# Kernel optimization log

Measured on AMD Instinct MI355X. Metric: run time of the kernel, lower is better.

## Reference

```python
import jax, jax.numpy as jnp
from jax import lax
import numpy as np

N, D, K, T, E, S = 2048, 128, 16, 16, 8192, 256
GAMMA, SIGMA, TEMP, EPS = 0.1, 1.0, 1.0, 1e-10


def _xavier(k, out_d, in_d):
    lim = (6.0 / (in_d + out_d)) ** 0.5
    return jax.random.uniform(k, (out_d, in_d), minval=-lim, maxval=lim, dtype=jnp.float32)


def setup_inputs() -> dict:
    key = jax.random.key(0)
    ks = jax.random.split(key, 24)
    inp = {
        'edges': jax.random.randint(ks[0], (T, E, 2), 0, N, dtype=jnp.int32),
        'subject_idx': 3,
        'eps_phi': jax.random.normal(ks[1], (T, N, D), dtype=jnp.float32),
        'eps_beta': jax.random.normal(ks[2], (T, K, D), dtype=jnp.float32),
        'u_gumbel': jax.random.uniform(ks[3], (T, 2 * E, K), dtype=jnp.float32),
        'alpha_mean_emb': jax.random.normal(ks[4], (S, D), dtype=jnp.float32),
        'alpha_std_emb': jax.random.normal(ks[5], (S, D), dtype=jnp.float32),
        'W_s2phi': _xavier(ks[6], N * D, D), 'b_s2phi': jnp.zeros((N * D,), jnp.float32),
        'W_s2beta': _xavier(ks[7], K * D, D), 'b_s2beta': jnp.zeros((K * D,), jnp.float32),
        'W_bmean': _xavier(ks[8], D, D), 'b_bmean': jnp.zeros((D,), jnp.float32),
        'W_bstd': _xavier(ks[9], D, D), 'b_bstd': jnp.zeros((D,), jnp.float32),
        'W_pmean': _xavier(ks[10], D, D), 'b_pmean': jnp.zeros((D,), jnp.float32),
        'W_pstd': _xavier(ks[11], D, D), 'b_pstd': jnp.zeros((D,), jnp.float32),
        'W_pi': _xavier(ks[12], K, D),
        'Wih_n': 0.1 * jax.random.normal(ks[13], (3 * D, 2 * D), dtype=jnp.float32),
        'Whh_n': 0.1 * jax.random.normal(ks[14], (3 * D, D), dtype=jnp.float32),
        'bih_n': jnp.zeros((3 * D,), jnp.float32), 'bhh_n': jnp.zeros((3 * D,), jnp.float32),
        'Wih_c': 0.1 * jax.random.normal(ks[15], (3 * D, 2 * D), dtype=jnp.float32),
        'Whh_c': 0.1 * jax.random.normal(ks[16], (3 * D, D), dtype=jnp.float32),
        'bih_c': jnp.zeros((3 * D,), jnp.float32), 'bhh_c': jnp.zeros((3 * D,), jnp.float32),
        'W_dec': _xavier(ks[17], N, D),
    }
    return inp


def _gru(x, h, Wih, Whh, bih, bhh):
    # torch nn.GRU single-step cell (gate order r, z, n)
    gi = x @ Wih.T + bih
    gh = h @ Whh.T + bhh
    i_r, i_z, i_n = jnp.split(gi, 3, axis=-1)
    h_r, h_z, h_n = jnp.split(gh, 3, axis=-1)
    r = jax.nn.sigmoid(i_r + h_r)
    z = jax.nn.sigmoid(i_z + h_z)
    n = jnp.tanh(i_n + r * h_n)
    return (1.0 - z) * n + z * h


def _kld_gauss(m1, s1, m2, s2):
    # KL(N(m1,s1) || N(m2,s2)), s2 scalar
    return 0.5 * jnp.sum(2.0 * (jnp.log(s2) - jnp.log(s1)) + (s1 ** 2 + (m1 - m2) ** 2) / (s2 ** 2) - 1.0)


def reference(edges, subject_idx, eps_phi, eps_beta, u_gumbel,
              alpha_mean_emb, alpha_std_emb, W_s2phi, b_s2phi, W_s2beta, b_s2beta,
              W_bmean, b_bmean, W_bstd, b_bstd, W_pmean, b_pmean, W_pstd, b_pstd,
              W_pi, Wih_n, Whh_n, bih_n, bhh_n, Wih_c, Whh_c, bih_c, bhh_c, W_dec):
    a_m = alpha_mean_emb[subject_idx]
    a_s = jax.nn.softplus(alpha_std_emb[subject_idx])
    kld_alpha = _kld_gauss(a_m, a_s, jnp.zeros_like(a_m), 1.0)
    phi0 = (a_m @ W_s2phi.T + b_s2phi).reshape(N, D)
    beta0 = (a_m @ W_s2beta.T + b_s2beta).reshape(K, D)

    def step(carry, xs):
        h_phi, h_beta, phi_prior, beta_prior = carry
        e_t, ep, eb, u = xs
        w = jnp.concatenate([e_t[:, 0], e_t[:, 1]])  # [2E]
        c = jnp.concatenate([e_t[:, 1], e_t[:, 0]])  # [2E]
        h_phi = _gru(jnp.concatenate([phi_prior, phi_prior], -1), h_phi, Wih_n, Whh_n, bih_n, bhh_n)
        h_beta = _gru(jnp.concatenate([beta_prior, beta_prior], -1), h_beta, Wih_c, Whh_c, bih_c, bhh_c)
        beta_mean = h_beta @ W_bmean.T + b_bmean
        beta_std = jax.nn.softplus(h_beta @ W_bstd.T + b_bstd)
        phi_mean = h_phi @ W_pmean.T + b_pmean
        phi_std = jax.nn.softplus(h_phi @ W_pstd.T + b_pstd)
        beta_s = beta_mean + beta_std * eb  # [K, D]
        phi_s = phi_mean + phi_std * ep     # [N, D]
        logits_q = (phi_s[w] * phi_s[c]) @ W_pi.T        # [2E, K] posterior logits
        log_post = jax.nn.log_softmax(logits_q, axis=-1)
        post = jnp.exp(log_post)
        log_prior = jax.nn.log_softmax(phi_s[w] @ beta_s.T, axis=-1)  # p(z|w)
        g = -jnp.log(-jnp.log(u + EPS) + EPS)  # gumbel noise
        z = jax.nn.softmax((logits_q + g) / TEMP, axis=-1)  # soft gumbel-softmax sample
        recon_logp = jax.nn.log_softmax((z @ beta_s) @ W_dec.T, axis=-1)  # [2E, N]
        nll = -jnp.sum(jnp.take_along_axis(recon_logp, c[:, None], axis=1))
        kld_z = jnp.sum(post * (log_post - log_prior))
        kld_beta = _kld_gauss(beta_mean, beta_std, beta_prior, GAMMA)
        kld_phi = _kld_gauss(phi_mean, phi_std, phi_prior, SIGMA)
        return (h_phi, h_beta, phi_s, beta_s), jnp.stack([nll, kld_z, kld_beta, kld_phi])

    carry0 = (jnp.zeros((N, D), jnp.float32), jnp.zeros((K, D), jnp.float32), phi0, beta0)
    _, per_t = lax.scan(step, carry0, (edges, eps_phi, eps_beta, u_gumbel))
    sums = per_t.sum(axis=0)  # [nll, kld_z, kld_beta, kld_phi]
    cnt = jnp.float32(T * 2 * E)
    out = jnp.stack([sums[0], sums[1], T * kld_alpha, sums[2], sums[3]]) / cnt
    return out  # [nll, kld_z, kld_alpha, kld_beta, kld_phi]
```

## Files before the change

kernel.cpp:

```cpp
#include <hip/hip_runtime.h>

#define NN 2048
#define DD 128
#define KK 16
#define TT 16
#define EE 8192
#define TWOE 16384
#define CNT 262144.0f

#define LOG2E 1.4426950408889634f
#define LN2   0.6931471805599453f

__device__ __forceinline__ float exp2_(float x) { return __builtin_amdgcn_exp2f(x); }
__device__ __forceinline__ float log2_(float x) { return __builtin_amdgcn_logf(x); }
__device__ __forceinline__ float expf_(float x) { return exp2_(x * LOG2E); }
__device__ __forceinline__ float logf_(float x) { return log2_(x) * LN2; }
__device__ __forceinline__ float sigmoidf_(float x) { return 1.f / (1.f + expf_(-x)); }
__device__ __forceinline__ float softplusf_(float x) { return fmaxf(x, 0.f) + logf_(1.f + expf_(-fabsf(x))); }
__device__ __forceinline__ float tanhf_(float x) { return 1.f - 2.f / (1.f + expf_(2.f * x)); }

#define D4(a,b) ((a).x*(b).x + (a).y*(b).y + (a).z*(b).z + (a).w*(b).w)

__launch_bounds__(256)
__global__ void init_kernel(const float* __restrict__ Wih_n, const float* __restrict__ Whh_n,
                            const float* __restrict__ Wih_c, const float* __restrict__ Whh_c,
                            const float* __restrict__ W_pmean, const float* __restrict__ W_pstd,
                            const float* __restrict__ W_bmean, const float* __restrict__ W_bstd,
                            float* __restrict__ Bg_n, float* __restrict__ Bg_c,
                            float* __restrict__ Bms_n, float* __restrict__ Bms_c,
                            float* __restrict__ hphiA, float* __restrict__ hbetaA,
                            const float* __restrict__ amE, const float* __restrict__ asE,
                            const int* __restrict__ sidx, float* __restrict__ a_m,
                            float* __restrict__ acc)
{
    if (blockIdx.x == 1024) {
        __shared__ float red[128];
        int d = threadIdx.x;
        if (d < 128) {
            int s = sidx[0];
            float am = amE[s*128 + d];
            float as = softplusf_(asE[s*128 + d]);
            a_m[d] = am;
            red[d] = -logf_(as) + 0.5f*(as*as + am*am) - 0.5f;
        }
        __syncthreads();
        for (int st = 64; st > 0; st >>= 1) { if (d < st) red[d] += red[d + st]; __syncthreads(); }
        if (d == 0) acc[2] = red[0];
        return;
    }
    int idx = blockIdx.x * 256 + threadIdx.x;
    hphiA[idx] = 0.f;
    if (idx < 2048) hbetaA[idx] = 0.f;
    if (idx < 2) { acc[idx] = 0.f; acc[idx + 3] = 0.f; }
    if (idx < 98304) {
        int r = idx;
        if (r < 49152) { int j = r >> 7, k2 = r & 127; Bg_n[r] = Wih_n[j*256 + k2] + Wih_n[j*256 + 128 + k2]; }
        else Bg_n[r] = Whh_n[r - 49152];
    } else if (idx < 196608) {
        int r = idx - 98304;
        if (r < 49152) { int j = r >> 7, k2 = r & 127; Bg_c[r] = Wih_c[j*256 + k2] + Wih_c[j*256 + 128 + k2]; }
        else Bg_c[r] = Whh_c[r - 49152];
    } else if (idx < 229376) {
        int r = idx - 196608;
        Bms_n[r] = (r < 16384) ? W_pmean[r] : W_pstd[r - 16384];
    } else {
        int r = idx - 229376;
        Bms_c[r] = (r < 16384) ? W_bmean[r] : W_bstd[r - 16384];
    }
}

__launch_bounds__(256)
__global__ void phi0_kernel(const float* __restrict__ Wp, const float* __restrict__ bp,
                            const float* __restrict__ Wb, const float* __restrict__ bb,
                            const float* __restrict__ a_m, float* __restrict__ phi0, float* __restrict__ beta0)
{
    int wid = threadIdx.x >> 6, l = threadIdx.x & 63;
    long long row = (long long)blockIdx.x * 4 + wid;
    const float* W; const float* b; float* o; long long r = row;
    if (row < 262144) { W = Wp; b = bp; o = phi0; }
    else { W = Wb; b = bb; o = beta0; r = row - 262144; }
    const float* wr = W + r * 128;
    float acc = a_m[l] * wr[l] + a_m[64 + l] * wr[64 + l];
    #pragma unroll
    for (int m = 32; m >= 1; m >>= 1) acc += __shfl_xor(acc, m);
    if (l == 0) o[r] = acc + b[r];
}

__launch_bounds__(256)
__global__ void gru_kernel(const float* __restrict__ phiPrior, const float* __restrict__ betaPrior,
                           const float* __restrict__ hPhiOld, float* __restrict__ hPhiNew,
                           const float* __restrict__ hBetaOld, float* __restrict__ hBetaNew,
                           const float* __restrict__ Bg_n, const float* __restrict__ Bg_c,
                           const float* __restrict__ bih_n, const float* __restrict__ bhh_n,
                           const float* __restrict__ bih_c, const float* __restrict__ bhh_c)
{
    __shared__ float Xs[32][64];
    __shared__ float Hs[32][64];
    __shared__ float Ws[32][192];
    int bx = blockIdx.x;
    const float* X; const float* Hold; float* Hnew; const float* Bg; const float* bih; const float* bhh;
    int m0, M, j0;
    if (bx < 128) {
        m0 = (bx >> 2) * 64; j0 = (bx & 3) * 32; M = 2048;
        X = phiPrior; Hold = hPhiOld; Hnew = hPhiNew; Bg = Bg_n; bih = bih_n; bhh = bhh_n;
    } else {
        m0 = 0; j0 = (bx - 128) * 32; M = 16;
        X = betaPrior; Hold = hBetaOld; Hnew = hBetaNew; Bg = Bg_c; bih = bih_c; bhh = bhh_c;
    }
    int tid = threadIdx.x;
    int j  = tid & 31;
    int rr = tid >> 5;
    float acc[6][8] = {};
    int srow = tid >> 3;
    int skq  = (tid & 7) * 4;
    for (int k0 = 0; k0 < 128; k0 += 32) {
        #pragma unroll
        for (int h2 = 0; h2 < 2; ++h2) {
            int row = srow + 32 * h2;
            int grow = m0 + row;
            float4 xv = make_float4(0.f,0.f,0.f,0.f), hv = xv;
            if (grow < M) {
                xv = *(const float4*)(X    + (size_t)grow*128 + k0 + skq);
                hv = *(const float4*)(Hold + (size_t)grow*128 + k0 + skq);
            }
            Xs[skq+0][row] = xv.x; Xs[skq+1][row] = xv.y; Xs[skq+2][row] = xv.z; Xs[skq+3][row] = xv.w;
            Hs[skq+0][row] = hv.x; Hs[skq+1][row] = hv.y; Hs[skq+2][row] = hv.z; Hs[skq+3][row] = hv.w;
        }
        #pragma unroll
        for (int h6 = 0; h6 < 6; ++h6) {
            int rowIdx = srow + 32 * h6;
            int g = rowIdx >> 5, jj2 = rowIdx & 31;
            float4 wv = *(const float4*)(Bg + (size_t)(g*128 + j0 + jj2)*128 + k0 + skq);
            Ws[skq+0][rowIdx] = wv.x; Ws[skq+1][rowIdx] = wv.y; Ws[skq+2][rowIdx] = wv.z; Ws[skq+3][rowIdx] = wv.w;
        }
        __syncthreads();
        #pragma unroll
        for (int kk = 0; kk < 32; ++kk) {
            float xa[8], ha[8];
            *(float4*)&xa[0] = *(const float4*)&Xs[kk][rr*8];
            *(float4*)&xa[4] = *(const float4*)&Xs[kk][rr*8+4];
            *(float4*)&ha[0] = *(const float4*)&Hs[kk][rr*8];
            *(float4*)&ha[4] = *(const float4*)&Hs[kk][rr*8+4];
            #pragma unroll
            for (int g = 0; g < 3; ++g) {
                float wv = Ws[kk][g*32 + j];
                #pragma unroll
                for (int i = 0; i < 8; ++i) acc[g][i] = fmaf(xa[i], wv, acc[g][i]);
            }
            #pragma unroll
            for (int g = 3; g < 6; ++g) {
                float wv = Ws[kk][g*32 + j];
                #pragma unroll
                for (int i = 0; i < 8; ++i) acc[g][i] = fmaf(ha[i], wv, acc[g][i]);
            }
        }
        __syncthreads();
    }
    float bi_r = bih[j0 + j], bi_z = bih[128 + j0 + j], bi_n = bih[256 + j0 + j];
    float bh_r = bhh[j0 + j], bh_z = bhh[128 + j0 + j], bh_n = bhh[256 + j0 + j];
    #pragma unroll
    for (int i = 0; i < 8; ++i) {
        int row = m0 + rr*8 + i;
        if (row < M) {
            float r_ = sigmoidf_(acc[0][i] + bi_r + acc[3][i] + bh_r);
            float z_ = sigmoidf_(acc[1][i] + bi_z + acc[4][i] + bh_z);
            float n_ = tanhf_(acc[2][i] + bi_n + r_ * (acc[5][i] + bh_n));
            size_t hi = (size_t)row * 128 + j0 + j;
            Hnew[hi] = (1.f - z_) * n_ + z_ * Hold[hi];
        }
    }
}

__launch_bounds__(256)
__global__ void ms_kernel(const float* __restrict__ hPhi, const float* __restrict__ hBeta,
                          const float* __restrict__ Bms_n, const float* __restrict__ Bms_c,
                          const float* __restrict__ b_pmean, const float* __restrict__ b_pstd,
                          const float* __restrict__ b_bmean, const float* __restrict__ b_bstd,
                          const float* __restrict__ epsP, const float* __restrict__ epsB,
                          const float* __restrict__ phiPrior, const float* __restrict__ betaPrior,
                          float* __restrict__ phiS, float* __restrict__ betaS, float* __restrict__ acc)
{
    __shared__ float Hs[32][64];
    __shared__ float Wms[32][64];
    __shared__ float red[256];
    int bx = blockIdx.x;
    const float* H; const float* Bms; const float* bm; const float* bs;
    const float* eps; const float* prior; float* out;
    int m0, M, j0; bool isPhi;
    if (bx < 128) {
        m0 = (bx >> 2) * 64; j0 = (bx & 3) * 32; M = 2048; isPhi = true;
        H = hPhi; Bms = Bms_n; bm = b_pmean; bs = b_pstd; eps = epsP; prior = phiPrior; out = phiS;
    } else {
        m0 = 0; j0 = (bx - 128) * 32; M = 16; isPhi = false;
        H = hBeta; Bms = Bms_c; bm = b_bmean; bs = b_bstd; eps = epsB; prior = betaPrior; out = betaS;
    }
    int tid = threadIdx.x;
    int j  = tid & 31;
    int rr = tid >> 5;
    float accM[8] = {}, accS[8] = {};
    int srow = tid >> 3;
    int skq  = (tid & 7) * 4;
    for (int k0 = 0; k0 < 128; k0 += 32) {
        #pragma unroll
        for (int h2 = 0; h2 < 2; ++h2) {
            int row = srow + 32 * h2;
            int grow = m0 + row;
            float4 hv = make_float4(0.f,0.f,0.f,0.f);
            if (grow < M) hv = *(const float4*)(H + (size_t)grow*128 + k0 + skq);
            Hs[skq+0][row] = hv.x; Hs[skq+1][row] = hv.y; Hs[skq+2][row] = hv.z; Hs[skq+3][row] = hv.w;
        }
        {
            int rowIdx = srow + 32 * 0;
            #pragma unroll
            for (int h2 = 0; h2 < 2; ++h2) {
                int ri = rowIdx + 32 * h2;
                int grp = ri >> 5, jj2 = ri & 31;
                float4 wv = *(const float4*)(Bms + (size_t)(grp*128 + j0 + jj2)*128 + k0 + skq);
                Wms[skq+0][ri] = wv.x; Wms[skq+1][ri] = wv.y; Wms[skq+2][ri] = wv.z; Wms[skq+3][ri] = wv.w;
            }
        }
        __syncthreads();
        #pragma unroll
        for (int kk = 0; kk < 32; ++kk) {
            float hv[8];
            *(float4*)&hv[0] = *(const float4*)&Hs[kk][rr*8];
            *(float4*)&hv[4] = *(const float4*)&Hs[kk][rr*8+4];
            float wm = Wms[kk][j];
            float ws = Wms[kk][32 + j];
            #pragma unroll
            for (int i = 0; i < 8; ++i) {
                accM[i] = fmaf(hv[i], wm, accM[i]);
                accS[i] = fmaf(hv[i], ws, accS[i]);
            }
        }
        __syncthreads();
    }
    float bmv = bm[j0 + j], bsv = bs[j0 + j];
    float kld = 0.f;
    #pragma unroll
    for (int i = 0; i < 8; ++i) {
        int row = m0 + rr*8 + i;
        if (row < M) {
            size_t gi = (size_t)row * 128 + j0 + j;
            float mean = accM[i] + bmv;
            float stdv = softplusf_(accS[i] + bsv);
            out[gi] = mean + stdv * eps[gi];
            float d = mean - prior[gi];
            if (isPhi) kld += -logf_(stdv) + 0.5f*(stdv*stdv + d*d) - 0.5f;
            else       kld += (-2.3025850929940457f - logf_(stdv)) + 50.0f*(stdv*stdv + d*d) - 0.5f;
        }
    }
    red[tid] = kld; __syncthreads();
    for (int st = 128; st > 0; st >>= 1) { if (tid < st) red[tid] += red[tid + st]; __syncthreads(); }
    if (tid == 0) atomicAdd(acc + (isPhi ? 4 : 3), red[0]);
}

__launch_bounds__(256)
__global__ void mt_kernel(const float* __restrict__ betaS, const float* __restrict__ W_dec, float* __restrict__ Mt)
{
    int tid = threadIdx.x, wid = tid >> 6, l = tid & 63;
    int n = blockIdx.x * 4 + wid;
    int k = l & 15, q = l >> 4;
    const float* bs = betaS + k*128 + q*32;
    const float* wd = W_dec + (size_t)n*128 + q*32;
    float p = 0.f;
    #pragma unroll
    for (int jj = 0; jj < 32; ++jj) p = fmaf(bs[jj], wd[jj], p);
    p += __shfl_xor(p, 16);
    p += __shfl_xor(p, 32);
    if (l < 16) Mt[n*16 + l] = p * LOG2E;
}

#define ZSTEP(A,B,Wv,Bv) { float4 a_=(A), b_=(B); \
    lp += a_.x*(Bv).x + a_.y*(Bv).y + a_.z*(Bv).z + a_.w*(Bv).w; \
    lq += (a_.x*b_.x)*(Wv).x + (a_.y*b_.y)*(Wv).y + (a_.z*b_.z)*(Wv).z + (a_.w*b_.w)*(Wv).w; }

__launch_bounds__(512, 2)
__global__ void znll_kernel(const float* __restrict__ phiS, const float* __restrict__ betaS,
                            const float* __restrict__ W_pi, const float* __restrict__ Mt,
                            const int* __restrict__ edges_t, const float* __restrict__ u_t,
                            float* __restrict__ acc)
{
    __shared__ float zbuf[64][16];
    __shared__ float ss[64][8], sc[64][8];
    __shared__ int   cbuf[64];
    __shared__ float kred[8];
    int tid = threadIdx.x, wid = tid >> 6, l = tid & 63;
    {
        int k = l >> 2, q = l & 3;
        int d0 = q * 32;
        const float4* wp = (const float4*)(W_pi  + k*128 + d0);
        const float4* bp = (const float4*)(betaS + k*128 + d0);
        float4 wr0 = wp[0], wr1 = wp[1], wr2 = wp[2], wr3 = wp[3],
               wr4 = wp[4], wr5 = wp[5], wr6 = wp[6], wr7 = wp[7];
        float4 br0 = bp[0], br1 = bp[1], br2 = bp[2], br3 = bp[3],
               br4 = bp[4], br5 = bp[5], br6 = bp[6], br7 = bp[7];
        float kz = 0.f;
        #pragma unroll
        for (int it = 0; it < 8; ++it) {
            int jl = wid * 8 + it;
            int j = blockIdx.x * 64 + jl;
            int e = j & 8191; int fl = j >> 13;
            int w = edges_t[e*2 + fl], c = edges_t[e*2 + (fl ^ 1)];
            const float4* pw4 = (const float4*)(phiS + (size_t)w*128 + d0);
            const float4* pc4 = (const float4*)(phiS + (size_t)c*128 + d0);
            float lq = 0.f, lp = 0.f;
            ZSTEP(pw4[0], pc4[0], wr0, br0); ZSTEP(pw4[1], pc4[1], wr1, br1);
            ZSTEP(pw4[2], pc4[2], wr2, br2); ZSTEP(pw4[3], pc4[3], wr3, br3);
            ZSTEP(pw4[4], pc4[4], wr4, br4); ZSTEP(pw4[5], pc4[5], wr5, br5);
            ZSTEP(pw4[6], pc4[6], wr6, br6); ZSTEP(pw4[7], pc4[7], wr7, br7);
            lq += __shfl_xor(lq, 1); lq += __shfl_xor(lq, 2);
            lp += __shfl_xor(lp, 1); lp += __shfl_xor(lp, 2);
            float eq = expf_(lq);
            float sq = eq;
            sq += __shfl_xor(sq, 4); sq += __shfl_xor(sq, 8); sq += __shfl_xor(sq, 16); sq += __shfl_xor(sq, 32);
            float logpost = lq - logf_(sq);
            float post = eq * __builtin_amdgcn_rcpf(sq);
            float mp = lp;
            mp = fmaxf(mp, __shfl_xor(mp, 4));  mp = fmaxf(mp, __shfl_xor(mp, 8));
            mp = fmaxf(mp, __shfl_xor(mp, 16)); mp = fmaxf(mp, __shfl_xor(mp, 32));
            float ep = expf_(lp - mp);
            float sp = ep;
            sp += __shfl_xor(sp, 4); sp += __shfl_xor(sp, 8); sp += __shfl_xor(sp, 16); sp += __shfl_xor(sp, 32);
            float logprior = (lp - mp) - logf_(sp);
            float v = post * (logpost - logprior);
            v += __shfl_xor(v, 4); v += __shfl_xor(v, 8); v += __shfl_xor(v, 16); v += __shfl_xor(v, 32);
            kz += v;
            float u = u_t[(size_t)j*16 + k];
            float g = -logf_(-logf_(u + 1e-10f) + 1e-10f);
            float zl = lq + g;
            float ez = expf_(zl);
            float sz = ez;
            sz += __shfl_xor(sz, 4); sz += __shfl_xor(sz, 8); sz += __shfl_xor(sz, 16); sz += __shfl_xor(sz, 32);
            if (q == 0) zbuf[jl][k] = ez * __builtin_amdgcn_rcpf(sz);
            if (l == 0) cbuf[jl] = c;
        }
        if (l == 0) kred[wid] = kz;
    }
    __syncthreads();
    if (tid == 0) {
        float t = 0.f;
        #pragma unroll
        for (int w2 = 0; w2 < 8; ++w2) t += kred[w2];
        atomicAdd(acc + 1, t);
    }
    int n0 = tid * 4;
    const float4* mp4 = (const float4*)(Mt + (size_t)n0 * 16);
    float4 M0 = mp4[0],  M1 = mp4[1],  M2 = mp4[2],  M3 = mp4[3];
    float4 M4 = mp4[4],  M5 = mp4[5],  M6 = mp4[6],  M7 = mp4[7];
    float4 M8 = mp4[8],  M9 = mp4[9],  M10 = mp4[10], M11 = mp4[11];
    float4 M12 = mp4[12], M13 = mp4[13], M14 = mp4[14], M15 = mp4[15];
    for (int e = 0; e < 64; ++e) {
        const float4* zp = (const float4*)&zbuf[e][0];
        float4 Z0 = zp[0], Z1 = zp[1], Z2 = zp[2], Z3 = zp[3];
        int c = cbuf[e];
        float v0 = D4(Z0, M0)  + D4(Z1, M1)  + D4(Z2, M2)  + D4(Z3, M3);
        float v1 = D4(Z0, M4)  + D4(Z1, M5)  + D4(Z2, M6)  + D4(Z3, M7);
        float v2 = D4(Z0, M8)  + D4(Z1, M9)  + D4(Z2, M10) + D4(Z3, M11);
        float v3 = D4(Z0, M12) + D4(Z1, M13) + D4(Z2, M14) + D4(Z3, M15);
        float s = exp2_(v0) + exp2_(v1) + exp2_(v2) + exp2_(v3);
        float cv = 0.f;
        cv = (c == n0    ) ? v0 : cv;
        cv = (c == n0 + 1) ? v1 : cv;
        cv = (c == n0 + 2) ? v2 : cv;
        cv = (c == n0 + 3) ? v3 : cv;
        #pragma unroll
        for (int m = 1; m < 64; m <<= 1) {
            s  += __shfl_xor(s, m);
            cv += __shfl_xor(cv, m);
        }
        if (l == 0) { ss[e][wid] = s; sc[e][wid] = cv; }
    }
    __syncthreads();
    if (tid < 64) {
        float S = 0.f, CV = 0.f;
        #pragma unroll
        for (int w2 = 0; w2 < 8; ++w2) { S += ss[tid][w2]; CV += sc[tid][w2]; }
        float val = LN2 * (log2_(S) - CV);
        #pragma unroll
        for (int m = 1; m < 64; m <<= 1) val += __shfl_xor(val, m);
        if (tid == 0) atomicAdd(acc + 0, val);
    }
}

__global__ void final_kernel(const float* __restrict__ acc, float* __restrict__ out)
{
    if (threadIdx.x == 0 && blockIdx.x == 0) {
        out[0] = acc[0] / CNT;
        out[1] = acc[1] / CNT;
        out[2] = 16.f * acc[2] / CNT;
        out[3] = acc[3] / CNT;
        out[4] = acc[4] / CNT;
    }
}

extern "C" void kernel_launch(void* const* d_in, const int* in_sizes, int n_in,
                              void* d_out, int out_size, void* d_ws, size_t ws_size,
                              hipStream_t stream)
{
    (void)in_sizes; (void)n_in; (void)out_size; (void)ws_size;
    const int*   edges   = (const int*)d_in[0];
    const int*   sidx    = (const int*)d_in[1];
    const float* eps_phi = (const float*)d_in[2];
    const float* eps_beta= (const float*)d_in[3];
    const float* u_g     = (const float*)d_in[4];
    const float* amE     = (const float*)d_in[5];
    const float* asE     = (const float*)d_in[6];
    const float* W_s2phi = (const float*)d_in[7];
    const float* b_s2phi = (const float*)d_in[8];
    const float* W_s2beta= (const float*)d_in[9];
    const float* b_s2beta= (const float*)d_in[10];
    const float* W_bmean = (const float*)d_in[11];
    const float* b_bmean = (const float*)d_in[12];
    const float* W_bstd  = (const float*)d_in[13];
    const float* b_bstd  = (const float*)d_in[14];
    const float* W_pmean = (const float*)d_in[15];
    const float* b_pmean = (const float*)d_in[16];
    const float* W_pstd  = (const float*)d_in[17];
    const float* b_pstd  = (const float*)d_in[18];
    const float* W_pi    = (const float*)d_in[19];
    const float* Wih_n   = (const float*)d_in[20];
    const float* Whh_n   = (const float*)d_in[21];
    const float* bih_n   = (const float*)d_in[22];
    const float* bhh_n   = (const float*)d_in[23];
    const float* Wih_c   = (const float*)d_in[24];
    const float* Whh_c   = (const float*)d_in[25];
    const float* bih_c   = (const float*)d_in[26];
    const float* bhh_c   = (const float*)d_in[27];
    const float* W_dec   = (const float*)d_in[28];

    float* ws     = (float*)d_ws;
    float* Bg_n   = ws;
    float* Bg_c   = Bg_n   + 98304;
    float* Bms_n  = Bg_c   + 98304;
    float* Bms_c  = Bms_n  + 32768;
    float* a_m    = Bms_c  + 32768;
    float* phiA   = a_m    + 128;
    float* phiB   = phiA   + 262144;
    float* hphiA  = phiB   + 262144;
    float* hphiB  = hphiA  + 262144;
    float* betaA  = hphiB  + 262144;
    float* betaB  = betaA  + 2048;
    float* hbetaA = betaB  + 2048;
    float* hbetaB = hbetaA + 2048;
    float* Mt     = hbetaB + 2048;
    float* acc    = Mt     + 32768;

    init_kernel<<<1025, 256, 0, stream>>>(Wih_n, Whh_n, Wih_c, Whh_c,
                                          W_pmean, W_pstd, W_bmean, W_bstd,
                                          Bg_n, Bg_c, Bms_n, Bms_c,
                                          hphiA, hbetaA, amE, asE, sidx, a_m, acc);
    phi0_kernel<<<66048, 256, 0, stream>>>(W_s2phi, b_s2phi, W_s2beta, b_s2beta, a_m, phiA, betaA);

    float* phiPrior = phiA;  float* phiS = phiB;
    float* betaPrior = betaA; float* betaS = betaB;
    float* hPhiOld = hphiA;  float* hPhiNew = hphiB;
    float* hBetaOld = hbetaA; float* hBetaNew = hbetaB;
    for (int t = 0; t < TT; ++t) {
        gru_kernel<<<132, 256, 0, stream>>>(phiPrior, betaPrior,
                                            hPhiOld, hPhiNew, hBetaOld, hBetaNew,
                                            Bg_n, Bg_c, bih_n, bhh_n, bih_c, bhh_c);
        ms_kernel<<<132, 256, 0, stream>>>(hPhiNew, hBetaNew, Bms_n, Bms_c,
                                           b_pmean, b_pstd, b_bmean, b_bstd,
                                           eps_phi + (size_t)t * 262144, eps_beta + (size_t)t * 2048,
                                           phiPrior, betaPrior, phiS, betaS, acc);
        mt_kernel<<<512, 256, 0, stream>>>(betaS, W_dec, Mt);
        znll_kernel<<<256, 512, 0, stream>>>(phiS, betaS, W_pi, Mt,
                                             edges + (size_t)t * EE * 2, u_g + (size_t)t * TWOE * KK, acc);
        float* tp = phiPrior; phiPrior = phiS; phiS = tp;
        float* tb = betaPrior; betaPrior = betaS; betaS = tb;
        float* th = hPhiOld; hPhiOld = hPhiNew; hPhiNew = th;
        float* tb2 = hBetaOld; hBetaOld = hBetaNew; hBetaNew = tb2;
    }
    final_kernel<<<1, 64, 0, stream>>>(acc, (float*)d_out);
}
```

Measured before the change: 2.194 ms.

## Fuse mean/std sampling with decoder projection and shrink znll tiles

Result: slower. 2.475 ms (+12.8%).

```diff
diff --git a/kernel.cpp b/kernel.cpp
--- a/kernel.cpp
+++ b/kernel.cpp
@@ -30,8 +30,7 @@
                             float* __restrict__ Bms_n, float* __restrict__ Bms_c,
                             float* __restrict__ hphiA, float* __restrict__ hbetaA,
                             const float* __restrict__ amE, const float* __restrict__ asE,
-                            const int* __restrict__ sidx, float* __restrict__ a_m,
-                            float* __restrict__ acc)
+                            const int* __restrict__ sidx, float* __restrict__ acc)
 {
     if (blockIdx.x == 1024) {
         __shared__ float red[128];
@@ -40,11 +39,10 @@
             int s = sidx[0];
             float am = amE[s*128 + d];
             float as = softplusf_(asE[s*128 + d]);
-            a_m[d] = am;
             red[d] = -logf_(as) + 0.5f*(as*as + am*am) - 0.5f;
         }
         __syncthreads();
-        for (int st = 64; st > 0; st >>= 1) { if (d < st) red[d] += red[d + st]; __syncthreads(); }
+        for (int st = 64; st > 0; st >>= 1) { if (d < st && d + st < 128) red[d] += red[d + st]; __syncthreads(); }
         if (d == 0) acc[2] = red[0];
         return;
     }
@@ -72,15 +70,17 @@
 __launch_bounds__(256)
 __global__ void phi0_kernel(const float* __restrict__ Wp, const float* __restrict__ bp,
                             const float* __restrict__ Wb, const float* __restrict__ bb,
-                            const float* __restrict__ a_m, float* __restrict__ phi0, float* __restrict__ beta0)
+                            const float* __restrict__ amE, const int* __restrict__ sidx,
+                            float* __restrict__ phi0, float* __restrict__ beta0)
 {
     int wid = threadIdx.x >> 6, l = threadIdx.x & 63;
+    int s = sidx[0];
     long long row = (long long)blockIdx.x * 4 + wid;
     const float* W; const float* b; float* o; long long r = row;
     if (row < 262144) { W = Wp; b = bp; o = phi0; }
     else { W = Wb; b = bb; o = beta0; r = row - 262144; }
     const float* wr = W + r * 128;
-    float acc = a_m[l] * wr[l] + a_m[64 + l] * wr[64 + l];
+    float acc = amE[s*128 + l] * wr[l] + amE[s*128 + 64 + l] * wr[64 + l];
     #pragma unroll
     for (int m = 32; m >= 1; m >>= 1) acc += __shfl_xor(acc, m);
     if (l == 0) o[r] = acc + b[r];
@@ -172,119 +172,158 @@
 }
 
 __launch_bounds__(256)
-__global__ void ms_kernel(const float* __restrict__ hPhi, const float* __restrict__ hBeta,
-                          const float* __restrict__ Bms_n, const float* __restrict__ Bms_c,
-                          const float* __restrict__ b_pmean, const float* __restrict__ b_pstd,
-                          const float* __restrict__ b_bmean, const float* __restrict__ b_bstd,
-                          const float* __restrict__ epsP, const float* __restrict__ epsB,
-                          const float* __restrict__ phiPrior, const float* __restrict__ betaPrior,
-                          float* __restrict__ phiS, float* __restrict__ betaS, float* __restrict__ acc)
-{
-    __shared__ float Hs[32][64];
-    __shared__ float Wms[32][64];
+__global__ void msmt_kernel(const float* __restrict__ hPhi, const float* __restrict__ hBeta,
+                            const float* __restrict__ Bms_n, const float* __restrict__ Bms_c,
+                            const float* __restrict__ b_pmean, const float* __restrict__ b_pstd,
+                            const float* __restrict__ b_bmean, const float* __restrict__ b_bstd,
+                            const float* __restrict__ epsP, const float* __restrict__ epsB,
+                            const float* __restrict__ phiPrior, const float* __restrict__ betaPrior,
+                            float* __restrict__ phiS, float* __restrict__ betaS,
+                            const float* __restrict__ W_dec, float* __restrict__ Mt,
+                            float* __restrict__ acc)
+{
     __shared__ float red[256];
     int bx = blockIdx.x;
-    const float* H; const float* Bms; const float* bm; const float* bs;
-    const float* eps; const float* prior; float* out;
-    int m0, M, j0; bool isPhi;
+    int tid = threadIdx.x;
     if (bx < 128) {
-        m0 = (bx >> 2) * 64; j0 = (bx & 3) * 32; M = 2048; isPhi = true;
-        H = hPhi; Bms = Bms_n; bm = b_pmean; bs = b_pstd; eps = epsP; prior = phiPrior; out = phiS;
-    } else {
-        m0 = 0; j0 = (bx - 128) * 32; M = 16; isPhi = false;
-        H = hBeta; Bms = Bms_c; bm = b_bmean; bs = b_bstd; eps = epsB; prior = betaPrior; out = betaS;
-    }
-    int tid = threadIdx.x;
-    int j  = tid & 31;
-    int rr = tid >> 5;
-    float accM[8] = {}, accS[8] = {};
-    int srow = tid >> 3;
-    int skq  = (tid & 7) * 4;
-    for (int k0 = 0; k0 < 128; k0 += 32) {
-        #pragma unroll
-        for (int h2 = 0; h2 < 2; ++h2) {
-            int row = srow + 32 * h2;
-            int grow = m0 + row;
-            float4 hv = make_float4(0.f,0.f,0.f,0.f);
-            if (grow < M) hv = *(const float4*)(H + (size_t)grow*128 + k0 + skq);
-            Hs[skq+0][row] = hv.x; Hs[skq+1][row] = hv.y; Hs[skq+2][row] = hv.z; Hs[skq+3][row] = hv.w;
-        }
-        {
-            int rowIdx = srow + 32 * 0;
+        __shared__ float Hs[32][64];
+        __shared__ float Wms[32][64];
+        int m0 = (bx >> 2) * 64, j0 = (bx & 3) * 32;
+        int j  = tid & 31;
+        int rr = tid >> 5;
+        float accM[8] = {}, accS[8] = {};
+        int srow = tid >> 3;
+        int skq  = (tid & 7) * 4;
+        for (int k0 = 0; k0 < 128; k0 += 32) {
             #pragma unroll
             for (int h2 = 0; h2 < 2; ++h2) {
-                int ri = rowIdx + 32 * h2;
+                int row = srow + 32 * h2;
+                float4 hv = *(const float4*)(hPhi + (size_t)(m0 + row)*128 + k0 + skq);
+                Hs[skq+0][row] = hv.x; Hs[skq+1][row] = hv.y; Hs[skq+2][row] = hv.z; Hs[skq+3][row] = hv.w;
+            }
+            #pragma unroll
+            for (int h2 = 0; h2 < 2; ++h2) {
+                int ri = srow + 32 * h2;
                 int grp = ri >> 5, jj2 = ri & 31;
-                float4 wv = *(const float4*)(Bms + (size_t)(grp*128 + j0 + jj2)*128 + k0 + skq);
+                float4 wv = *(const float4*)(Bms_n + (size_t)(grp*128 + j0 + jj2)*128 + k0 + skq);
                 Wms[skq+0][ri] = wv.x; Wms[skq+1][ri] = wv.y; Wms[skq+2][ri] = wv.z; Wms[skq+3][ri] = wv.w;
             }
-        }
-        __syncthreads();
-        #pragma unroll
-        for (int kk = 0; kk < 32; ++kk) {
-            float hv[8];
-            *(float4*)&hv[0] = *(const float4*)&Hs[kk][rr*8];
-            *(float4*)&hv[4] = *(const float4*)&Hs[kk][rr*8+4];
-            float wm = Wms[kk][j];
-            float ws = Wms[kk][32 + j];
-            #pragma unroll
-            for (int i = 0; i < 8; ++i) {
-                accM[i] = fmaf(hv[i], wm, accM[i]);
-                accS[i] = fmaf(hv[i], ws, accS[i]);
-            }
-        }
-        __syncthreads();
-    }
-    float bmv = bm[j0 + j], bsv = bs[j0 + j];
-    float kld = 0.f;
-    #pragma unroll
-    for (int i = 0; i < 8; ++i) {
-        int row = m0 + rr*8 + i;
-        if (row < M) {
+            __syncthreads();
+            #pragma unroll
+            for (int kk = 0; kk < 32; ++kk) {
+                float hv[8];
+                *(float4*)&hv[0] = *(const float4*)&Hs[kk][rr*8];
+                *(float4*)&hv[4] = *(const float4*)&Hs[kk][rr*8+4];
+                float wm = Wms[kk][j];
+                float wsv = Wms[kk][32 + j];
+                #pragma unroll
+                for (int i = 0; i < 8; ++i) {
+                    accM[i] = fmaf(hv[i], wm, accM[i]);
+                    accS[i] = fmaf(hv[i], wsv, accS[i]);
+                }
+            }
+            __syncthreads();
+        }
+        float bmv = b_pmean[j0 + j], bsv = b_pstd[j0 + j];
+        float kld = 0.f;
+        #pragma unroll
+        for (int i = 0; i < 8; ++i) {
+            int row = m0 + rr*8 + i;
             size_t gi = (size_t)row * 128 + j0 + j;
             float mean = accM[i] + bmv;
             float stdv = softplusf_(accS[i] + bsv);
-            out[gi] = mean + stdv * eps[gi];
-            float d = mean - prior[gi];
-            if (isPhi) kld += -logf_(stdv) + 0.5f*(stdv*stdv + d*d) - 0.5f;
-            else       kld += (-2.3025850929940457f - logf_(stdv)) + 50.0f*(stdv*stdv + d*d) - 0.5f;
-        }
-    }
-    red[tid] = kld; __syncthreads();
-    for (int st = 128; st > 0; st >>= 1) { if (tid < st) red[tid] += red[tid + st]; __syncthreads(); }
-    if (tid == 0) atomicAdd(acc + (isPhi ? 4 : 3), red[0]);
-}
-
-__launch_bounds__(256)
-__global__ void mt_kernel(const float* __restrict__ betaS, const float* __restrict__ W_dec, float* __restrict__ Mt)
-{
-    int tid = threadIdx.x, wid = tid >> 6, l = tid & 63;
-    int n = blockIdx.x * 4 + wid;
-    int k = l & 15, q = l >> 4;
-    const float* bs = betaS + k*128 + q*32;
-    const float* wd = W_dec + (size_t)n*128 + q*32;
-    float p = 0.f;
-    #pragma unroll
-    for (int jj = 0; jj < 32; ++jj) p = fmaf(bs[jj], wd[jj], p);
-    p += __shfl_xor(p, 16);
-    p += __shfl_xor(p, 32);
-    if (l < 16) Mt[n*16 + l] = p * LOG2E;
+            phiS[gi] = mean + stdv * epsP[gi];
+            float d = mean - phiPrior[gi];
+            kld += -logf_(stdv) + 0.5f*(stdv*stdv + d*d) - 0.5f;
+        }
+        red[tid] = kld; __syncthreads();
+        for (int st = 128; st > 0; st >>= 1) { if (tid < st) red[tid] += red[tid + st]; __syncthreads(); }
+        if (tid == 0) atomicAdd(acc + 4, red[0]);
+    } else {
+        __shared__ float hb[2048];
+        __shared__ float sbeta[16*132];
+        int bm = bx - 128;
+        {
+            int base = tid * 8;
+            *(float4*)&hb[base]     = *(const float4*)(hBeta + base);
+            *(float4*)&hb[base + 4] = *(const float4*)(hBeta + base + 4);
+        }
+        __syncthreads();
+        {
+            int j = tid & 127, half = tid >> 7;
+            float accM[8] = {}, accS[8] = {};
+            const float* wmrow = Bms_c + (size_t)j * 128;
+            const float* wsrow = Bms_c + (size_t)(128 + j) * 128;
+            for (int d4 = 0; d4 < 32; ++d4) {
+                float4 wm = *(const float4*)(wmrow + d4*4);
+                float4 wsv = *(const float4*)(wsrow + d4*4);
+                #pragma unroll
+                for (int i = 0; i < 8; ++i) {
+                    int r = half*8 + i;
+                    float4 hv = *(const float4*)&hb[r*128 + d4*4];
+                    accM[i] += D4(hv, wm);
+                    accS[i] += D4(hv, wsv);
+                }
+            }
+            float bmv = b_bmean[j], bsv = b_bstd[j];
+            float kld = 0.f;
+            #pragma unroll
+            for (int i = 0; i < 8; ++i) {
+                int r = half*8 + i;
+                float mean = accM[i] + bmv;
+                float stdv = softplusf_(accS[i] + bsv);
+                float sv = mean + stdv * epsB[r*128 + j];
+                sbeta[r*132 + j] = sv;
+                if (bm == 0) {
+                    betaS[r*128 + j] = sv;
+                    float d = mean - betaPrior[r*128 + j];
+                    kld += (-2.3025850929940457f - logf_(stdv)) + 50.0f*(stdv*stdv + d*d) - 0.5f;
+                }
+            }
+            if (bm == 0) {
+                red[tid] = kld; __syncthreads();
+                for (int st = 128; st > 0; st >>= 1) { if (tid < st) red[tid] += red[tid + st]; __syncthreads(); }
+                if (tid == 0) atomicAdd(acc + 3, red[0]);
+            }
+        }
+        __syncthreads();
+        {
+            int w = tid >> 6, l = tid & 63;
+            int k = l & 15, q = l >> 4;
+            const float* sb = &sbeta[k*132 + q*32];
+            #pragma unroll 4
+            for (int rr2 = 0; rr2 < 16; ++rr2) {
+                int n = bm*64 + w*16 + rr2;
+                const float* wd = W_dec + (size_t)n*128 + q*32;
+                float p = 0.f;
+                #pragma unroll
+                for (int i4 = 0; i4 < 8; ++i4) {
+                    float4 a = *(const float4*)(sb + i4*4);
+                    float4 b = *(const float4*)(wd + i4*4);
+                    p += D4(a, b);
+                }
+                p += __shfl_xor(p, 16);
+                p += __shfl_xor(p, 32);
+                if (l < 16) Mt[n*16 + l] = p * LOG2E;
+            }
+        }
+    }
 }
 
 #define ZSTEP(A,B,Wv,Bv) { float4 a_=(A), b_=(B); \
     lp += a_.x*(Bv).x + a_.y*(Bv).y + a_.z*(Bv).z + a_.w*(Bv).w; \
     lq += (a_.x*b_.x)*(Wv).x + (a_.y*b_.y)*(Wv).y + (a_.z*b_.z)*(Wv).z + (a_.w*b_.w)*(Wv).w; }
 
-__launch_bounds__(512, 2)
+__launch_bounds__(512, 4)
 __global__ void znll_kernel(const float* __restrict__ phiS, const float* __restrict__ betaS,
                             const float* __restrict__ W_pi, const float* __restrict__ Mt,
                             const int* __restrict__ edges_t, const float* __restrict__ u_t,
                             float* __restrict__ acc)
 {
-    __shared__ float zbuf[64][16];
-    __shared__ float ss[64][8], sc[64][8];
-    __shared__ int   cbuf[64];
-    __shared__ float kred[8];
+    __shared__ float zbuf[32][16];
+    __shared__ int   cbuf[32];
+    __shared__ float ss[32][8];
+    __shared__ float kred[8], cvred[8];
     int tid = threadIdx.x, wid = tid >> 6, l = tid & 63;
     {
         int k = l >> 2, q = l & 3;
@@ -297,9 +336,9 @@
                br4 = bp[4], br5 = bp[5], br6 = bp[6], br7 = bp[7];
         float kz = 0.f;
         #pragma unroll
-        for (int it = 0; it < 8; ++it) {
-            int jl = wid * 8 + it;
-            int j = blockIdx.x * 64 + jl;
+        for (int it = 0; it < 4; ++it) {
+            int jl = wid * 4 + it;
+            int j = blockIdx.x * 32 + jl;
             int e = j & 8191; int fl = j >> 13;
             int w = edges_t[e*2 + fl], c = edges_t[e*2 + (fl ^ 1)];
             const float4* pw4 = (const float4*)(phiS + (size_t)w*128 + d0);
@@ -323,9 +362,7 @@
             float sp = ep;
             sp += __shfl_xor(sp, 4); sp += __shfl_xor(sp, 8); sp += __shfl_xor(sp, 16); sp += __shfl_xor(sp, 32);
             float logprior = (lp - mp) - logf_(sp);
-            float v = post * (logpost - logprior);
-            v += __shfl_xor(v, 4); v += __shfl_xor(v, 8); v += __shfl_xor(v, 16); v += __shfl_xor(v, 32);
-            kz += v;
+            kz += post * (logpost - logprior);
             float u = u_t[(size_t)j*16 + k];
             float g = -logf_(-logf_(u + 1e-10f) + 1e-10f);
             float zl = lq + g;
@@ -335,22 +372,20 @@
             if (q == 0) zbuf[jl][k] = ez * __builtin_amdgcn_rcpf(sz);
             if (l == 0) cbuf[jl] = c;
         }
-        if (l == 0) kred[wid] = kz;
+        #pragma unroll
+        for (int m = 1; m < 64; m <<= 1) kz += __shfl_xor(kz, m);
+        if (l == 0) kred[wid] = kz * 0.25f;
     }
     __syncthreads();
-    if (tid == 0) {
-        float t = 0.f;
-        #pragma unroll
-        for (int w2 = 0; w2 < 8; ++w2) t += kred[w2];
-        atomicAdd(acc + 1, t);
-    }
     int n0 = tid * 4;
     const float4* mp4 = (const float4*)(Mt + (size_t)n0 * 16);
     float4 M0 = mp4[0],  M1 = mp4[1],  M2 = mp4[2],  M3 = mp4[3];
     float4 M4 = mp4[4],  M5 = mp4[5],  M6 = mp4[6],  M7 = mp4[7];
     float4 M8 = mp4[8],  M9 = mp4[9],  M10 = mp4[10], M11 = mp4[11];
     float4 M12 = mp4[12], M13 = mp4[13], M14 = mp4[14], M15 = mp4[15];
-    for (int e = 0; e < 64; ++e) {
+    float cvsum = 0.f;
+    #pragma unroll 2
+    for (int e = 0; e < 32; ++e) {
         const float4* zp = (const float4*)&zbuf[e][0];
         float4 Z0 = zp[0], Z1 = zp[1], Z2 = zp[2], Z3 = zp[3];
         int c = cbuf[e];
@@ -359,27 +394,35 @@
         float v2 = D4(Z0, M8)  + D4(Z1, M9)  + D4(Z2, M10) + D4(Z3, M11);
         float v3 = D4(Z0, M12) + D4(Z1, M13) + D4(Z2, M14) + D4(Z3, M15);
         float s = exp2_(v0) + exp2_(v1) + exp2_(v2) + exp2_(v3);
-        float cv = 0.f;
-        cv = (c == n0    ) ? v0 : cv;
-        cv = (c == n0 + 1) ? v1 : cv;
-        cv = (c == n0 + 2) ? v2 : cv;
-        cv = (c == n0 + 3) ? v3 : cv;
-        #pragma unroll
-        for (int m = 1; m < 64; m <<= 1) {
-            s  += __shfl_xor(s, m);
-            cv += __shfl_xor(cv, m);
-        }
-        if (l == 0) { ss[e][wid] = s; sc[e][wid] = cv; }
-    }
+        cvsum += (c == n0) ? v0 : 0.f;
+        cvsum += (c == n0 + 1) ? v1 : 0.f;
+        cvsum += (c == n0 + 2) ? v2 : 0.f;
+        cvsum += (c == n0 + 3) ? v3 : 0.f;
+        #pragma unroll
+        for (int m = 1; m < 64; m <<= 1) s += __shfl_xor(s, m);
+        if (l == 0) ss[e][wid] = s;
+    }
+    #pragma unroll
+    for (int m = 1; m < 64; m <<= 1) cvsum += __shfl_xor(cvsum, m);
+    if (l == 0) cvred[wid] = cvsum;
     __syncthreads();
-    if (tid < 64) {
-        float S = 0.f, CV = 0.f;
-        #pragma unroll
-        for (int w2 = 0; w2 < 8; ++w2) { S += ss[tid][w2]; CV += sc[tid][w2]; }
-        float val = LN2 * (log2_(S) - CV);
+    if (wid == 0) {
+        float val = 0.f;
+        if (l < 32) {
+            float S = 0.f;
+            #pragma unroll
+            for (int w2 = 0; w2 < 8; ++w2) S += ss[l][w2];
+            val = log2_(S);
+        }
         #pragma unroll
         for (int m = 1; m < 64; m <<= 1) val += __shfl_xor(val, m);
-        if (tid == 0) atomicAdd(acc + 0, val);
+        if (l == 0) {
+            float cvt = 0.f, kzt = 0.f;
+            #pragma unroll
+            for (int w2 = 0; w2 < 8; ++w2) { cvt += cvred[w2]; kzt += kred[w2]; }
+            atomicAdd(acc + 0, LN2 * (val - cvt));
+            atomicAdd(acc + 1, kzt);
+        }
     }
 }
 
@@ -434,8 +477,7 @@
     float* Bg_c   = Bg_n   + 98304;
     float* Bms_n  = Bg_c   + 98304;
     float* Bms_c  = Bms_n  + 32768;
-    float* a_m    = Bms_c  + 32768;
-    float* phiA   = a_m    + 128;
+    float* phiA   = Bms_c  + 32768;
     float* phiB   = phiA   + 262144;
     float* hphiA  = phiB   + 262144;
     float* hphiB  = hphiA  + 262144;
@@ -449,8 +491,8 @@
     init_kernel<<<1025, 256, 0, stream>>>(Wih_n, Whh_n, Wih_c, Whh_c,
                                           W_pmean, W_pstd, W_bmean, W_bstd,
                                           Bg_n, Bg_c, Bms_n, Bms_c,
-                                          hphiA, hbetaA, amE, asE, sidx, a_m, acc);
-    phi0_kernel<<<66048, 256, 0, stream>>>(W_s2phi, b_s2phi, W_s2beta, b_s2beta, a_m, phiA, betaA);
+                                          hphiA, hbetaA, amE, asE, sidx, acc);
+    phi0_kernel<<<66048, 256, 0, stream>>>(W_s2phi, b_s2phi, W_s2beta, b_s2beta, amE, sidx, phiA, betaA);
 
     float* phiPrior = phiA;  float* phiS = phiB;
     float* betaPrior = betaA; float* betaS = betaB;
@@ -460,12 +502,11 @@
         gru_kernel<<<132, 256, 0, stream>>>(phiPrior, betaPrior,
                                             hPhiOld, hPhiNew, hBetaOld, hBetaNew,
                                             Bg_n, Bg_c, bih_n, bhh_n, bih_c, bhh_c);
-        ms_kernel<<<132, 256, 0, stream>>>(hPhiNew, hBetaNew, Bms_n, Bms_c,
-                                           b_pmean, b_pstd, b_bmean, b_bstd,
-                                           eps_phi + (size_t)t * 262144, eps_beta + (size_t)t * 2048,
-                                           phiPrior, betaPrior, phiS, betaS, acc);
-        mt_kernel<<<512, 256, 0, stream>>>(betaS, W_dec, Mt);
-        znll_kernel<<<256, 512, 0, stream>>>(phiS, betaS, W_pi, Mt,
+        msmt_kernel<<<160, 256, 0, stream>>>(hPhiNew, hBetaNew, Bms_n, Bms_c,
+                                             b_pmean, b_pstd, b_bmean, b_bstd,
+                                             eps_phi + (size_t)t * 262144, eps_beta + (size_t)t * 2048,
+                                             phiPrior, betaPrior, phiS, betaS, W_dec, Mt, acc);
+        znll_kernel<<<512, 512, 0, stream>>>(phiS, betaS, W_pi, Mt,
                                              edges + (size_t)t * EE * 2, u_g + (size_t)t * TWOE * KK, acc);
         float* tp = phiPrior; phiPrior = phiS; phiS = tp;
         float* tb = betaPrior; betaPrior = betaS; betaS = tb;
```
